# Performance work log

Hardware: AMD Instinct MI355X
Metric: run time of the kernel (lower is better)

## Reference

```python
import jax, jax.numpy as jnp
import numpy as np

# static config
B, T, D, E, K = 2, 2048, 1024, 8, 2
CAPACITY_FACTOR = 1.25
NT = B * T  # num_tokens
_cap = K * NT / E * CAPACITY_FACTOR
_cap += _cap % 2
EXP_CAP = int(_cap)  # 1280


def setup_inputs() -> dict:
    key = jax.random.key(0)
    k1, k2 = jax.random.split(key)
    x = jax.random.normal(k1, (B, T, D), dtype=jnp.float32)
    w_router = jax.random.normal(k2, (E, D), dtype=jnp.float32) * 0.02
    return {"x": x, "w_router": w_router}


def reference(x, w_router):
    # router logits: (B,T,E)
    logits = jnp.einsum('btd,ed->bte', x, w_router)

    # top-k selection
    topk_logits, topk_idx = jax.lax.top_k(logits, K)  # (B,T,K)

    # softmax over only the top-k logits (others masked to -inf), matching
    # torch's full_like(-inf).scatter_(topk) then softmax
    in_topk = jax.nn.one_hot(topk_idx, E, dtype=logits.dtype).sum(axis=-2) > 0  # (B,T,E)
    masked = jnp.where(in_topk, logits, -jnp.inf)
    router_probs = jax.nn.softmax(masked, axis=-1)  # (B,T,E)

    # expert assignment mask: (K, NT, E)
    exp_mask = jax.nn.one_hot(topk_idx, E, dtype=jnp.int32)  # (B,T,K,E)
    exp_mask = exp_mask.reshape(NT, K, E).transpose(1, 0, 2)

    # rank of each token within its expert's buffer (priority: k=0 tokens first)
    rank = jnp.cumsum(exp_mask.reshape(K * NT, E), axis=0) - 1
    rank = rank.reshape(K, NT, E)

    # drop tokens that exceed expert capacity
    exp_mask = exp_mask * (rank < EXP_CAP).astype(jnp.int32)
    used_cap = jnp.sum(exp_mask, axis=(0, 1))  # (E,)

    # per-(k, token) slot index within the assigned expert's buffer
    slot = jnp.sum(exp_mask * rank, axis=-1)  # (K, NT) int

    probs_flat = router_probs.reshape(NT, E)
    exp_weights = exp_mask.astype(probs_flat.dtype) * probs_flat[None]  # (K,NT,E)

    # cb_weight[t, e, c] = sum_k exp_weights[k,t,e] * (slot[k,t] == c)
    # scatter-add instead of materializing the one-hot (K,NT,EXP_CAP) tensor
    t_idx = jnp.broadcast_to(jnp.arange(NT)[None, :], (K, NT))
    cb_weight = jnp.zeros((NT, E, EXP_CAP), dtype=probs_flat.dtype)
    cb_weight = cb_weight.at[t_idx, :, slot].add(exp_weights)  # (NT,E,EXP_CAP)

    sec_mask = cb_weight != 0  # bool dispatch mask
    return used_cap, cb_weight, sec_mask
```

## Files before the change

### kernel.cpp

```cpp
#include <hip/hip_runtime.h>
#include <hip/hip_bf16.h>
#include <math.h>

#define NT      4096
#define DD      1024
#define EE      8
#define KK      2
#define CAP     1280
#define CBN     (NT * EE * CAP)

#define NBL     64
#define NBZ     960
#define ZTOT    20971520ull

__device__ __forceinline__ int swz(int j) { return j ^ ((j >> 5) & 31); }

__global__ __launch_bounds__(256) void zero_logits_kernel(
    const float* __restrict__ x,
    const float* __restrict__ w,
    float* __restrict__ out,
    int* __restrict__ e0, int* __restrict__ e1,
    float* __restrict__ p0, float* __restrict__ p1)
{
    __shared__ float wl[EE * DD];

    if (blockIdx.x >= NBL) {
        const float4 zv = make_float4(0.f, 0.f, 0.f, 0.f);
        float4* dst = reinterpret_cast<float4*>(out + 8);
        size_t i = (size_t)(blockIdx.x - NBL) * 256 + threadIdx.x;
        const size_t stride = (size_t)NBZ * 256;
        for (; i < ZTOT; i += stride) dst[i] = zv;
        return;
    }

    for (int i = threadIdx.x; i < EE * DD / 4; i += 256)
        reinterpret_cast<float4*>(wl)[i] = reinterpret_cast<const float4*>(w)[i];
    __syncthreads();

    const int wave = threadIdx.x >> 6;
    const int lane = threadIdx.x & 63;
    const int wid  = blockIdx.x * 4 + wave;

    for (int t = wid; t < NT; t += NBL * 4) {
        const float4* xt = reinterpret_cast<const float4*>(x + (size_t)t * DD);
        float acc[EE];
        #pragma unroll
        for (int e = 0; e < EE; ++e) acc[e] = 0.0f;

        #pragma unroll
        for (int ii = 0; ii < DD / 4 / 64; ++ii) {
            const int i = ii * 64 + lane;
            const float4 xv = xt[i];
            #pragma unroll
            for (int e = 0; e < EE; ++e) {
                const float4 wv = reinterpret_cast<const float4*>(wl + e * DD)[i];
                acc[e] += xv.x * wv.x + xv.y * wv.y + xv.z * wv.z + xv.w * wv.w;
            }
        }

        #pragma unroll
        for (int e = 0; e < EE; ++e) {
            float v = acc[e];
            #pragma unroll
            for (int off = 32; off > 0; off >>= 1) v += __shfl_xor(v, off);
            acc[e] = v;
        }

        if (lane == 0) {
            int b0 = 0; float l0 = acc[0];
            #pragma unroll
            for (int e = 1; e < EE; ++e) { if (acc[e] > l0) { l0 = acc[e]; b0 = e; } }
            int b1 = -1; float l1 = -INFINITY;
            #pragma unroll
            for (int e = 0; e < EE; ++e) { if (e != b0 && acc[e] > l1) { l1 = acc[e]; b1 = e; } }

            const float z  = expf(l1 - l0);
            const float pa = 1.0f / (1.0f + z);
            const float pb = z * pa;

            e0[t] = b0; e1[t] = b1;
            p0[t] = pa; p1[t] = pb;
        }
    }
}

__global__ __launch_bounds__(256) void rank_scatter_kernel(
    const int* __restrict__ e0, const int* __restrict__ e1,
    const float* __restrict__ p0, const float* __restrict__ p1,
    float* __restrict__ out)
{
    __shared__ int   se[KK * NT];
    __shared__ float sp[KK * NT];
    __shared__ unsigned long long wsumA[4], wsumB[4];

    const int tid = threadIdx.x;

    for (int i = tid; i < NT; i += 256) {
        se[swz(i)]      = e0[i];
        se[swz(NT + i)] = e1[i];
        sp[swz(i)]      = p0[i];
        sp[swz(NT + i)] = p1[i];
    }
    __syncthreads();

    const int base = tid * 32;
    unsigned long long ca = 0ull, cb = 0ull;
    #pragma unroll
    for (int i = 0; i < 32; ++i) {
        const int e = se[swz(base + i)];
        if (e < 4) ca += 1ull << (16 * e);
        else       cb += 1ull << (16 * (e - 4));
    }

    unsigned long long sa = ca, sb = cb;
    #pragma unroll
    for (int off = 1; off < 64; off <<= 1) {
        const unsigned long long ta = __shfl_up(sa, off);
        const unsigned long long tb = __shfl_up(sb, off);
        if ((tid & 63) >= off) { sa += ta; sb += tb; }
    }
    const int wv = tid >> 6;
    if ((tid & 63) == 63) { wsumA[wv] = sa; wsumB[wv] = sb; }
    __syncthreads();

    unsigned long long preA = 0ull, preB = 0ull;
    #pragma unroll
    for (int k = 0; k < 4; ++k) {
        if (k < wv) { preA += wsumA[k]; preB += wsumB[k]; }
    }
    unsigned long long ra = preA + sa - ca;
    unsigned long long rb = preB + sb - cb;

    #pragma unroll
    for (int i = 0; i < 32; ++i) {
        const int j = base + i;
        const int e = se[swz(j)];
        int rank;
        if (e < 4) { rank = (int)((ra >> (16 * e)) & 0xFFFF);       ra += 1ull << (16 * e); }
        else       { rank = (int)((rb >> (16 * (e - 4))) & 0xFFFF); rb += 1ull << (16 * (e - 4)); }
        if (rank < CAP) {
            const float p = sp[swz(j)];
            if (p != 0.0f) {
                const int t = j & (NT - 1);
                const size_t idx = (size_t)t * (EE * CAP) + (size_t)e * CAP + (size_t)rank;
                out[8 + idx] = p;
                out[8 + (size_t)CBN + idx] = 1.0f;
            }
        }
    }

    if (tid < EE) {
        const unsigned long long totA = wsumA[0] + wsumA[1] + wsumA[2] + wsumA[3];
        const unsigned long long totB = wsumB[0] + wsumB[1] + wsumB[2] + wsumB[3];
        const int e = tid;
        const int tot = (e < 4) ? (int)((totA >> (16 * e)) & 0xFFFF)
                                : (int)((totB >> (16 * (e - 4))) & 0xFFFF);
        out[e] = (float)((tot < CAP) ? tot : CAP);
    }
}

extern "C" void kernel_launch(void* const* d_in, const int* in_sizes, int n_in,
                              void* d_out, int out_size, void* d_ws, size_t ws_size,
                              hipStream_t stream) {
    const float* x = (const float*)d_in[0];
    const float* w = (const float*)d_in[1];
    float* out = (float*)d_out;

    char* ws = (char*)d_ws;
    int*   e0 = (int*)(ws);
    int*   e1 = (int*)(ws + 16 * 1024);
    float* p0 = (float*)(ws + 32 * 1024);
    float* p1 = (float*)(ws + 48 * 1024);

    zero_logits_kernel<<<NBL + NBZ, 256, 0, stream>>>(x, w, out, e0, e1, p0, p1);

    rank_scatter_kernel<<<1, 256, 0, stream>>>(e0, e1, p0, p1, out);
}
```

Before: 97.86 us.

## Replace zero-fill plus scatter with a dense one-pass write from a slot table

Before, the kernel zero-filled the full dispatch buffer alongside the logits blocks and then scattered nonzeros from one block. Now a single-block pass builds a per-(token,expert) slot/value table, and a separate dense kernel writes every float4 of both the weight and mask outputs. That removes the read-after-zero ordering and the serial single-block scatter into the large buffers. In exchange it adds a third launch and a dependency on the single-block rank kernel before the bulk write can start, which may remove the overlap the old zero-fill had with the logits work.

```diff
diff --git a/kernel.cpp b/kernel.cpp
--- a/kernel.cpp
+++ b/kernel.cpp
@@ -8,31 +8,20 @@
 #define KK      2
 #define CAP     1280
 #define CBN     (NT * EE * CAP)
-
-#define NBL     64
-#define NBZ     960
-#define ZTOT    20971520ull
+#define NROW    (NT * EE)
+#define F4ROW   (CAP / 4)
+#define CB_F4   (CBN / 4)
 
 __device__ __forceinline__ int swz(int j) { return j ^ ((j >> 5) & 31); }
 
-__global__ __launch_bounds__(256) void zero_logits_kernel(
+__global__ __launch_bounds__(256) void logits_kernel(
     const float* __restrict__ x,
     const float* __restrict__ w,
-    float* __restrict__ out,
     int* __restrict__ e0, int* __restrict__ e1,
     float* __restrict__ p0, float* __restrict__ p1)
 {
     __shared__ float wl[EE * DD];
 
-    if (blockIdx.x >= NBL) {
-        const float4 zv = make_float4(0.f, 0.f, 0.f, 0.f);
-        float4* dst = reinterpret_cast<float4*>(out + 8);
-        size_t i = (size_t)(blockIdx.x - NBL) * 256 + threadIdx.x;
-        const size_t stride = (size_t)NBZ * 256;
-        for (; i < ZTOT; i += stride) dst[i] = zv;
-        return;
-    }
-
     for (int i = threadIdx.x; i < EE * DD / 4; i += 256)
         reinterpret_cast<float4*>(wl)[i] = reinterpret_cast<const float4*>(w)[i];
     __syncthreads();
@@ -41,7 +30,7 @@
     const int lane = threadIdx.x & 63;
     const int wid  = blockIdx.x * 4 + wave;
 
-    for (int t = wid; t < NT; t += NBL * 4) {
+    for (int t = wid; t < NT; t += gridDim.x * 4) {
         const float4* xt = reinterpret_cast<const float4*>(x + (size_t)t * DD);
         float acc[EE];
         #pragma unroll
@@ -84,9 +73,10 @@
     }
 }
 
-__global__ __launch_bounds__(256) void rank_scatter_kernel(
+__global__ __launch_bounds__(256) void rank_table_kernel(
     const int* __restrict__ e0, const int* __restrict__ e1,
     const float* __restrict__ p0, const float* __restrict__ p1,
+    int* __restrict__ sl, float* __restrict__ val,
     float* __restrict__ out)
 {
     __shared__ int   se[KK * NT];
@@ -94,6 +84,10 @@
     __shared__ unsigned long long wsumA[4], wsumB[4];
 
     const int tid = threadIdx.x;
+
+    int4* sl4 = reinterpret_cast<int4*>(sl);
+    const int4 neg = make_int4(-1, -1, -1, -1);
+    for (int i = tid; i < NROW / 4; i += 256) sl4[i] = neg;
 
     for (int i = tid; i < NT; i += 256) {
         se[swz(i)]      = e0[i];
@@ -139,13 +133,9 @@
         if (e < 4) { rank = (int)((ra >> (16 * e)) & 0xFFFF);       ra += 1ull << (16 * e); }
         else       { rank = (int)((rb >> (16 * (e - 4))) & 0xFFFF); rb += 1ull << (16 * (e - 4)); }
         if (rank < CAP) {
-            const float p = sp[swz(j)];
-            if (p != 0.0f) {
-                const int t = j & (NT - 1);
-                const size_t idx = (size_t)t * (EE * CAP) + (size_t)e * CAP + (size_t)rank;
-                out[8 + idx] = p;
-                out[8 + (size_t)CBN + idx] = 1.0f;
-            }
+            const int t = j & (NT - 1);
+            sl[t * EE + e]  = rank;
+            val[t * EE + e] = sp[swz(j)];
         }
     }
 
@@ -159,6 +149,37 @@
     }
 }
 
+__global__ __launch_bounds__(256) void write_kernel(
+    const int* __restrict__ sl, const float* __restrict__ val,
+    float* __restrict__ out)
+{
+    float4* cb = reinterpret_cast<float4*>(out + 8);
+    float4* mk = reinterpret_cast<float4*>(out + 8 + (size_t)CBN);
+
+    int i = blockIdx.x * 256 + threadIdx.x;
+    const int stride = gridDim.x * 256;
+    for (; i < CB_F4; i += stride) {
+        const int r  = i / F4ROW;
+        const int c0 = (i - r * F4ROW) * 4;
+        const int s  = sl[r];
+        const float p = val[r];
+        const bool on = (p != 0.0f);
+
+        float4 v, m;
+        const bool h0 = on && (s == c0);
+        const bool h1 = on && (s == c0 + 1);
+        const bool h2 = on && (s == c0 + 2);
+        const bool h3 = on && (s == c0 + 3);
+        v.x = h0 ? p : 0.0f;  m.x = h0 ? 1.0f : 0.0f;
+        v.y = h1 ? p : 0.0f;  m.y = h1 ? 1.0f : 0.0f;
+        v.z = h2 ? p : 0.0f;  m.z = h2 ? 1.0f : 0.0f;
+        v.w = h3 ? p : 0.0f;  m.w = h3 ? 1.0f : 0.0f;
+
+        cb[i] = v;
+        mk[i] = m;
+    }
+}
+
 extern "C" void kernel_launch(void* const* d_in, const int* in_sizes, int n_in,
                               void* d_out, int out_size, void* d_ws, size_t ws_size,
                               hipStream_t stream) {
@@ -167,12 +188,16 @@
     float* out = (float*)d_out;
 
     char* ws = (char*)d_ws;
-    int*   e0 = (int*)(ws);
-    int*   e1 = (int*)(ws + 16 * 1024);
-    float* p0 = (float*)(ws + 32 * 1024);
-    float* p1 = (float*)(ws + 48 * 1024);
-
-    zero_logits_kernel<<<NBL + NBZ, 256, 0, stream>>>(x, w, out, e0, e1, p0, p1);
-
-    rank_scatter_kernel<<<1, 256, 0, stream>>>(e0, e1, p0, p1, out);
-}
+    int*   e0  = (int*)(ws);
+    int*   e1  = (int*)(ws + 16 * 1024);
+    float* p0  = (float*)(ws + 32 * 1024);
+    float* p1  = (float*)(ws + 48 * 1024);
+    int*   sl  = (int*)(ws + 64 * 1024);
+    float* val = (float*)(ws + 192 * 1024);
+
+    logits_kernel<<<256, 256, 0, stream>>>(x, w, e0, e1, p0, p1);
+
+    rank_table_kernel<<<1, 256, 0, stream>>>(e0, e1, p0, p1, sl, val, out);
+
+    write_kernel<<<2048, 256, 0, stream>>>(sl, val, out);
+}
```

Result: no change. 99.61 us (+1.8%).
